# Optimization experiments

Measured on AMD Instinct MI355X. Metric: run time of the kernel, lower is better.

## Reference

```python
import jax, jax.numpy as jnp
import numpy as np

P = 2    # padding
R = 2    # ref[0]: rows/cols gathered as conv channels
WP = 3   # ref[1]: conv kernel length along border


def setup_inputs() -> dict:
    key = jax.random.key(0)
    ks = jax.random.split(key, 8)
    B, C, H, W = 8, 128, 256, 256
    HID = 8
    x = jax.random.normal(ks[0], (B, C, H, W), dtype=jnp.float32)
    # stacked params for 4 border MLPs: order top, bottom, left, right
    w1 = jax.random.normal(ks[1], (4, HID, R, WP), dtype=jnp.float32) * 0.3
    b1 = jax.random.normal(ks[2], (4, HID), dtype=jnp.float32) * 0.1
    w2 = jax.random.normal(ks[3], (4, HID, HID), dtype=jnp.float32) * 0.3
    b2 = jax.random.normal(ks[4], (4, HID), dtype=jnp.float32) * 0.1
    w3 = jax.random.normal(ks[5], (4, 1, HID), dtype=jnp.float32) * 0.3
    b3 = jax.random.normal(ks[6], (4, 1), dtype=jnp.float32) * 0.1
    return {"x": x, "w1": w1, "b1": b1, "w2": w2, "b2": b2, "w3": w3, "b3": b3}


def _mlp(slab, w1, b1, w2, b2, w3, b3):
    # slab: (B, R, L, C) -- R gathered lines as channels, L border length, C image channels
    L = slab.shape[2]
    # valid conv along L with WP taps: windows (B, R, WP, L-WP+1, C)
    wins = jnp.stack([slab[:, :, k:L - WP + 1 + k, :] for k in range(WP)], axis=2)
    h = jax.nn.relu(jnp.einsum('brklc,hrk->bhlc', wins, w1) + b1[None, :, None, None])
    h = jax.nn.relu(jnp.einsum('bhlc,gh->bglc', h, w2) + b2[None, :, None, None])
    o = jax.nn.relu(jnp.einsum('bglc,og->bolc', h, w3) + b3[None, :, None, None])
    return o[:, 0]  # (B, L-2, C)


def reference(x, w1, b1, w2, b2, w3, b3):
    B, C, H, W = x.shape
    H2, W2 = H + 2 * P, W + 2 * P
    xp = jnp.zeros((B, C, H2, W2), x.dtype).at[:, :, P:H + P, P:W + P].set(x)
    for i in range(P):
        # top: gather rows [P-i, P-i+R), write row P-1-i, cols 1:W2-1
        top = _mlp(jnp.transpose(xp[:, :, P - i:P + R - i, :], (0, 2, 3, 1)),
                   w1[0], b1[0], w2[0], b2[0], w3[0], b3[0])  # (B, W2-2, C)
        xp = xp.at[:, :, P - 1 - i, 1:W2 - 1].set(jnp.transpose(top, (0, 2, 1)))
        # bottom
        bot = _mlp(jnp.transpose(xp[:, :, H2 - 1 - (R + P) + i:H2 - 1 - P + i, :], (0, 2, 3, 1)),
                   w1[1], b1[1], w2[1], b2[1], w3[1], b3[1])
        xp = xp.at[:, :, H + P + i, 1:W2 - 1].set(jnp.transpose(bot, (0, 2, 1)))
        # left: gather cols, transpose so cols act as channels
        lef = _mlp(jnp.transpose(xp[:, :, :, P - i:P + R - i], (0, 3, 2, 1)),
                   w1[2], b1[2], w2[2], b2[2], w3[2], b3[2])  # (B, H2-2, C)
        xp = xp.at[:, :, 1:H2 - 1, P - 1 - i].set(jnp.transpose(lef, (0, 2, 1)))
        # right
        rig = _mlp(jnp.transpose(xp[:, :, :, W2 - 1 - (R + P) + i:W2 - 1 - P + i], (0, 3, 2, 1)),
                   w1[3], b1[3], w2[3], b2[3], w3[3], b3[3])
        xp = xp.at[:, :, 1:H2 - 1, W + P + i].set(jnp.transpose(rig, (0, 2, 1)))
    return xp
```

## Files before the change

kernel.cpp:

```cpp
#include <hip/hip_runtime.h>


__device__ __forceinline__ int bmap(int r) { return r < 4 ? r : r - 251; }

template <int S>
__device__ __forceinline__ float mlp6(const float* __restrict__ v,
                                      const float* __restrict__ w1,
                                      const float* __restrict__ b1,
                                      const float* __restrict__ w2,
                                      const float* __restrict__ b2,
                                      const float* __restrict__ w3,
                                      const float* __restrict__ b3)
{
    const float* __restrict__ W1 = w1 + S * 48;
    const float* __restrict__ B1 = b1 + S * 8;
    const float* __restrict__ W2 = w2 + S * 64;
    const float* __restrict__ B2 = b2 + S * 8;
    const float* __restrict__ W3 = w3 + S * 8;
    const float  b3s = b3[S];

    float h1[8];
#pragma unroll
    for (int h = 0; h < 8; ++h) {
        float a = B1[h];
#pragma unroll
        for (int q = 0; q < 6; ++q) a = fmaf(v[q], W1[h * 6 + q], a);
        h1[h] = fmaxf(a, 0.f);
    }
    float h2[8];
#pragma unroll
    for (int g = 0; g < 8; ++g) {
        float a = B2[g];
#pragma unroll
        for (int h = 0; h < 8; ++h) a = fmaf(h1[h], W2[g * 8 + h], a);
        h2[g] = fmaxf(a, 0.f);
    }
    float o = b3s;
#pragma unroll
    for (int g = 0; g < 8; ++g) o = fmaf(h2[g], W3[g], o);
    return fmaxf(o, 0.f);
}

template <int S>
__device__ __forceinline__ void hstage(int it, int tid,
                                       float (*rowS)[260], float (*colS)[260],
                                       const float* __restrict__ w1, const float* __restrict__ b1,
                                       const float* __restrict__ w2, const float* __restrict__ b2,
                                       const float* __restrict__ w3, const float* __restrict__ b3)
{
    int rin0, rin1, rout;
    if (S == 0) { rin0 = 2 - it;   rin1 = 3 - it;   rout = 1 - it;   }
    else        { rin0 = 255 + it; rin1 = 256 + it; rout = 258 + it; }
    const int a0 = bmap(rin0), a1 = bmap(rin1), ao = bmap(rout);
    for (int j0 = tid; j0 < 258; j0 += 256) {
        int j = j0 + 1;
        float v[6];
        v[0] = rowS[a0][j - 1]; v[1] = rowS[a0][j]; v[2] = rowS[a0][j + 1];
        v[3] = rowS[a1][j - 1]; v[4] = rowS[a1][j]; v[5] = rowS[a1][j + 1];
        float o = mlp6<S>(v, w1, b1, w2, b2, w3, b3);
        rowS[ao][j] = o;
        if (j < 4 || j >= 255) colS[bmap(j)][rout] = o;
    }
}

template <int S>
__device__ __forceinline__ void vstage(int it, int tid,
                                       float (*rowS)[260], float (*colS)[260],
                                       const float* __restrict__ w1, const float* __restrict__ b1,
                                       const float* __restrict__ w2, const float* __restrict__ b2,
                                       const float* __restrict__ w3, const float* __restrict__ b3)
{
    int cin0, cin1, cout;
    if (S == 2) { cin0 = 2 - it;   cin1 = 3 - it;   cout = 1 - it;   }
    else        { cin0 = 255 + it; cin1 = 256 + it; cout = 258 + it; }
    const int a0 = bmap(cin0), a1 = bmap(cin1), ao = bmap(cout);
    for (int r0 = tid; r0 < 258; r0 += 256) {
        int r = r0 + 1;
        float v[6];
        v[0] = colS[a0][r - 1]; v[1] = colS[a0][r]; v[2] = colS[a0][r + 1];
        v[3] = colS[a1][r - 1]; v[4] = colS[a1][r]; v[5] = colS[a1][r + 1];
        float o = mlp6<S>(v, w1, b1, w2, b2, w3, b3);
        colS[ao][r] = o;
        if (r < 4 || r >= 255) rowS[bmap(r)][cout] = o;
    }
}

__global__ __launch_bounds__(256) void border_kernel(
    const float* __restrict__ x,
    const float* __restrict__ w1, const float* __restrict__ b1,
    const float* __restrict__ w2, const float* __restrict__ b2,
    const float* __restrict__ w3, const float* __restrict__ b3,
    float* __restrict__ out)
{
    const int tid = threadIdx.x;
    const int bc  = blockIdx.x;
    const float* xs = x + (size_t)bc * 65536;
    float*       os = out + (size_t)bc * 67600;

    __shared__ float rowS[9][260];
    __shared__ float colS[9][260];

    for (int idx = tid; idx < 9 * 260; idx += 256) {
        (&rowS[0][0])[idx] = 0.f;
        (&colS[0][0])[idx] = 0.f;
    }
    __syncthreads();

    for (int which = 0; which < 5; ++which) {
        int xr = which < 2 ? which : 251 + which;
        rowS[2 + which][2 + tid] = xs[xr * 256 + tid];
        colS[2 + which][2 + tid] = xs[tid * 256 + xr];
    }
    __syncthreads();

    for (int it = 0; it < 2; ++it) {
        hstage<0>(it, tid, rowS, colS, w1, b1, w2, b2, w3, b3);
        hstage<1>(it, tid, rowS, colS, w1, b1, w2, b2, w3, b3);
        __syncthreads();
        vstage<2>(it, tid, rowS, colS, w1, b1, w2, b2, w3, b3);
        vstage<3>(it, tid, rowS, colS, w1, b1, w2, b2, w3, b3);
        __syncthreads();
    }

    for (int idx = tid; idx < 4 * 260; idx += 256) {
        int w = idx / 260, cc = idx % 260;
        int rr = w < 2 ? w : 256 + w;
        os[(size_t)rr * 260 + cc] = rowS[bmap(rr)][cc];
    }
    for (int idx = tid; idx < 4 * 256; idx += 256) {
        int w = idx >> 8, r = (idx & 255) + 2;
        int cc = w < 2 ? w : 256 + w;
        os[(size_t)r * 260 + cc] = colS[bmap(cc)][r];
    }
}

__global__ __launch_bounds__(256) void assemble_kernel(const float* __restrict__ x,
                                                       float* out)
{
    const int bc = blockIdx.y;
    const float* xrowbase = x + (size_t)bc * 65536;
    float*       os       = out + (size_t)bc * 67600;

    int idx = blockIdx.x * 256 + threadIdx.x;
    int r   = idx / 65;
    int k   = idx - r * 65;

    float*       orow = os + (size_t)(r + 2) * 260;
    const float* xrow = xrowbase + (size_t)r * 256;

    float4 val;
    if (k == 0) {
        float2 b = *(const float2*)(orow);
        float2 a = *(const float2*)(xrow);
        val = make_float4(b.x, b.y, a.x, a.y);
    } else if (k == 64) {
        float2 a = *(const float2*)(xrow + 254);
        float2 b = *(const float2*)(orow + 258);
        val = make_float4(a.x, a.y, b.x, b.y);
    } else {
        float2 a = *(const float2*)(xrow + 4 * k - 2);
        float2 c = *(const float2*)(xrow + 4 * k);
        val = make_float4(a.x, a.y, c.x, c.y);
    }
    *(float4*)(orow + 4 * k) = val;
}

extern "C" void kernel_launch(void* const* d_in, const int* in_sizes, int n_in,
                              void* d_out, int out_size, void* d_ws, size_t ws_size,
                              hipStream_t stream)
{
    const float* x  = (const float*)d_in[0];
    const float* w1 = (const float*)d_in[1];
    const float* b1 = (const float*)d_in[2];
    const float* w2 = (const float*)d_in[3];
    const float* b2 = (const float*)d_in[4];
    const float* w3 = (const float*)d_in[5];
    const float* b3 = (const float*)d_in[6];
    float* out = (float*)d_out;

    border_kernel<<<1024, 256, 0, stream>>>(x, w1, b1, w2, b2, w3, b3, out);
    assemble_kernel<<<dim3(65, 1024), 256, 0, stream>>>(x, out);
}
```

Measured before the change: 147.0 us.

## Fuse border MLP and interior assembly into one kernel with nontemporal IO

Merges the border-computation kernel and the interior-copy kernel into a single launch with 512 threads per block. Each block now also copies the interior rows of its channel, taking the border columns straight from shared memory instead of re-reading them from global memory. Global interior loads and stores use nontemporal hints. This removes a second launch and a global round trip for the border columns, but the whole copy now runs at one block per channel, which can limit parallelism across the GPU.

```diff
diff --git a/kernel.cpp b/kernel.cpp
--- a/kernel.cpp
+++ b/kernel.cpp
@@ -1,16 +1,16 @@
 #include <hip/hip_runtime.h>
 
+
+typedef float f32x4 __attribute__((ext_vector_type(4)));
+typedef float f32x2 __attribute__((ext_vector_type(2)));
 
 __device__ __forceinline__ int bmap(int r) { return r < 4 ? r : r - 251; }
 
 template <int S>
-__device__ __forceinline__ float mlp6(const float* __restrict__ v,
-                                      const float* __restrict__ w1,
-                                      const float* __restrict__ b1,
-                                      const float* __restrict__ w2,
-                                      const float* __restrict__ b2,
-                                      const float* __restrict__ w3,
-                                      const float* __restrict__ b3)
+__device__ __forceinline__ float mlp6(const float* v,
+                                      const float* __restrict__ w1, const float* __restrict__ b1,
+                                      const float* __restrict__ w2, const float* __restrict__ b2,
+                                      const float* __restrict__ w3, const float* __restrict__ b3)
 {
     const float* __restrict__ W1 = w1 + S * 48;
     const float* __restrict__ B1 = b1 + S * 8;
@@ -52,7 +52,7 @@
     if (S == 0) { rin0 = 2 - it;   rin1 = 3 - it;   rout = 1 - it;   }
     else        { rin0 = 255 + it; rin1 = 256 + it; rout = 258 + it; }
     const int a0 = bmap(rin0), a1 = bmap(rin1), ao = bmap(rout);
-    for (int j0 = tid; j0 < 258; j0 += 256) {
+    for (int j0 = tid; j0 < 258; j0 += 512) {
         int j = j0 + 1;
         float v[6];
         v[0] = rowS[a0][j - 1]; v[1] = rowS[a0][j]; v[2] = rowS[a0][j + 1];
@@ -74,7 +74,7 @@
     if (S == 2) { cin0 = 2 - it;   cin1 = 3 - it;   cout = 1 - it;   }
     else        { cin0 = 255 + it; cin1 = 256 + it; cout = 258 + it; }
     const int a0 = bmap(cin0), a1 = bmap(cin1), ao = bmap(cout);
-    for (int r0 = tid; r0 < 258; r0 += 256) {
+    for (int r0 = tid; r0 < 258; r0 += 512) {
         int r = r0 + 1;
         float v[6];
         v[0] = colS[a0][r - 1]; v[1] = colS[a0][r]; v[2] = colS[a0][r + 1];
@@ -85,7 +85,7 @@
     }
 }
 
-__global__ __launch_bounds__(256) void border_kernel(
+__global__ __launch_bounds__(512, 8) void fused_kernel(
     const float* __restrict__ x,
     const float* __restrict__ w1, const float* __restrict__ b1,
     const float* __restrict__ w2, const float* __restrict__ b2,
@@ -100,16 +100,21 @@
     __shared__ float rowS[9][260];
     __shared__ float colS[9][260];
 
-    for (int idx = tid; idx < 9 * 260; idx += 256) {
+    for (int idx = tid; idx < 9 * 260; idx += 512) {
         (&rowS[0][0])[idx] = 0.f;
         (&colS[0][0])[idx] = 0.f;
     }
     __syncthreads();
 
-    for (int which = 0; which < 5; ++which) {
+    for (int idx = tid; idx < 5 * 256; idx += 512) {
+        int which = idx >> 8, t = idx & 255;
         int xr = which < 2 ? which : 251 + which;
-        rowS[2 + which][2 + tid] = xs[xr * 256 + tid];
-        colS[2 + which][2 + tid] = xs[tid * 256 + xr];
+        rowS[2 + which][2 + t] = xs[xr * 256 + t];
+    }
+    for (int idx = tid; idx < 5 * 256; idx += 512) {
+        int which = idx >> 8, t = idx & 255;
+        int xr = which < 2 ? which : 251 + which;
+        colS[2 + which][2 + t] = xs[t * 256 + xr];
     }
     __syncthreads();
 
@@ -122,47 +127,31 @@
         __syncthreads();
     }
 
-    for (int idx = tid; idx < 4 * 260; idx += 256) {
+    for (int idx = tid; idx < 4 * 260; idx += 512) {
         int w = idx / 260, cc = idx % 260;
         int rr = w < 2 ? w : 256 + w;
-        os[(size_t)rr * 260 + cc] = rowS[bmap(rr)][cc];
+        __builtin_nontemporal_store(rowS[bmap(rr)][cc], &os[(size_t)rr * 260 + cc]);
     }
-    for (int idx = tid; idx < 4 * 256; idx += 256) {
-        int w = idx >> 8, r = (idx & 255) + 2;
-        int cc = w < 2 ? w : 256 + w;
-        os[(size_t)r * 260 + cc] = colS[bmap(cc)][r];
+
+    for (int idx = tid; idx < 256 * 65; idx += 512) {
+        int r = idx / 65;
+        int k = idx - r * 65;
+        int rp = r + 2;
+        float* orow = os + (size_t)rp * 260;
+        const float* xrow = xs + (size_t)r * 256;
+
+        f32x4 val;
+        if (k == 0) {
+            val = (f32x4){colS[0][rp], colS[1][rp], colS[2][rp], colS[3][rp]};
+        } else if (k == 64) {
+            val = (f32x4){colS[5][rp], colS[6][rp], colS[7][rp], colS[8][rp]};
+        } else {
+            f32x2 a = __builtin_nontemporal_load((const f32x2*)(xrow + 4 * k - 2));
+            f32x2 c = __builtin_nontemporal_load((const f32x2*)(xrow + 4 * k));
+            val = (f32x4){a.x, a.y, c.x, c.y};
+        }
+        __builtin_nontemporal_store(val, (f32x4*)(orow + 4 * k));
     }
-}
-
-__global__ __launch_bounds__(256) void assemble_kernel(const float* __restrict__ x,
-                                                       float* out)
-{
-    const int bc = blockIdx.y;
-    const float* xrowbase = x + (size_t)bc * 65536;
-    float*       os       = out + (size_t)bc * 67600;
-
-    int idx = blockIdx.x * 256 + threadIdx.x;
-    int r   = idx / 65;
-    int k   = idx - r * 65;
-
-    float*       orow = os + (size_t)(r + 2) * 260;
-    const float* xrow = xrowbase + (size_t)r * 256;
-
-    float4 val;
-    if (k == 0) {
-        float2 b = *(const float2*)(orow);
-        float2 a = *(const float2*)(xrow);
-        val = make_float4(b.x, b.y, a.x, a.y);
-    } else if (k == 64) {
-        float2 a = *(const float2*)(xrow + 254);
-        float2 b = *(const float2*)(orow + 258);
-        val = make_float4(a.x, a.y, b.x, b.y);
-    } else {
-        float2 a = *(const float2*)(xrow + 4 * k - 2);
-        float2 c = *(const float2*)(xrow + 4 * k);
-        val = make_float4(a.x, a.y, c.x, c.y);
-    }
-    *(float4*)(orow + 4 * k) = val;
 }
 
 extern "C" void kernel_launch(void* const* d_in, const int* in_sizes, int n_in,
@@ -178,6 +167,5 @@
     const float* b3 = (const float*)d_in[6];
     float* out = (float*)d_out;
 
-    border_kernel<<<1024, 256, 0, stream>>>(x, w1, b1, w2, b2, w3, b3, out);
-    assemble_kernel<<<dim3(65, 1024), 256, 0, stream>>>(x, out);
+    fused_kernel<<<1024, 512, 0, stream>>>(x, w1, b1, w2, b2, w3, b3, out);
 }
```

Result: faster. 140.1 us (-4.7%).
